# Kernel tuning notes

Measured on AMD Instinct MI355X. Metric: run time of the kernel, lower is better.

## Reference

```python
import jax, jax.numpy as jnp
import numpy as np


def _gaussian_orthogonal_random_matrix(nb_rows, nb_cols, seed=0):
    rng = np.random.default_rng(seed)
    blocks = []
    n_full = nb_rows // nb_cols
    for _ in range(n_full):
        q, _ = np.linalg.qr(rng.standard_normal((nb_cols, nb_cols)).astype(np.float64))
        blocks.append(q.T)
    rem = nb_rows - n_full * nb_cols
    if rem > 0:
        q, _ = np.linalg.qr(rng.standard_normal((nb_cols, nb_cols)).astype(np.float64))
        blocks.append(q.T[:rem])
    final = np.concatenate(blocks, axis=0)
    # scaling == 0: row multipliers are norms of gaussian rows
    multiplier = np.linalg.norm(rng.standard_normal((nb_rows, nb_cols)), axis=1)
    return (multiplier[:, None] * final).astype(np.float32)


def setup_inputs() -> dict:
    key = jax.random.key(0)
    kq, kk, kv = jax.random.split(key, 3)
    B, H, N, D = 4, 16, 4096, 64
    M = 256  # nb_features
    return {
        "q": jax.random.normal(kq, (B, H, N, D), dtype=jnp.float32),
        "k": jax.random.normal(kk, (B, H, N, D), dtype=jnp.float32),
        "v": jax.random.normal(kv, (B, H, N, D), dtype=jnp.float32),
        "projection_matrix": jnp.asarray(_gaussian_orthogonal_random_matrix(M, D)),
    }


def _softmax_kernel(data, proj, is_query, eps=1e-4):
    # data: [b,h,n,d], proj: [m,d]
    d = data.shape[-1]
    m = proj.shape[0]
    data_normalizer = d ** -0.25
    ratio = m ** -0.5
    data_dash = jnp.einsum('bhnd,md->bhnm', data_normalizer * data, proj)
    diag_data = jnp.sum(data * data, axis=-1, keepdims=True) * 0.5 * (data_normalizer ** 2)
    if is_query:
        mx = jnp.max(data_dash, axis=-1, keepdims=True)
    else:
        mx = jnp.max(data_dash, axis=(-2, -1), keepdims=True)
    mx = jax.lax.stop_gradient(mx)
    return ratio * (jnp.exp(data_dash - diag_data - mx) + eps)


def _linear_attention(q, k, v):
    # q,k: [b,h,n,m]; v: [b,h,n,e]
    k_cumsum = k.sum(axis=-2)                              # [b,h,m]
    d_inv = 1.0 / jnp.einsum('bhnm,bhm->bhn', q, k_cumsum)  # [b,h,n]
    context = jnp.einsum('bhnm,bhne->bhme', k, v)          # [b,h,m,e]
    return jnp.einsum('bhme,bhnm,bhn->bhne', context, q, d_inv)


def reference(q, k, v, projection_matrix):
    qp = _softmax_kernel(q, projection_matrix, is_query=True)
    kp = _softmax_kernel(k, projection_matrix, is_query=False)
    return _linear_attention(qp, kp, v)
```

## Files before the change

### kernel.cpp

```cpp
#include <hip/hip_runtime.h>
#include <math.h>

#define NSEQ  4096
#define DDIM  64
#define GH    64
#define NORMC 0.35355339059327373f
#define EPSC  1e-4f

typedef __bf16 bf16x8 __attribute__((ext_vector_type(8)));
typedef unsigned short u16x8 __attribute__((ext_vector_type(8)));
typedef float f32x4 __attribute__((ext_vector_type(4)));

__device__ __forceinline__ unsigned enc_f(float f) {
    unsigned b = __float_as_uint(f);
    return (b & 0x80000000u) ? ~b : (b | 0x80000000u);
}
__device__ __forceinline__ float dec_f(unsigned u) {
    return (u & 0x80000000u) ? __uint_as_float(u & 0x7FFFFFFFu) : __uint_as_float(~u);
}
__device__ __forceinline__ void split_hl(float f, unsigned short& h, unsigned short& l) {
    unsigned u = __float_as_uint(f);
    unsigned hb = u & 0xffff0000u;
    h = (unsigned short)(hb >> 16);
    l = (unsigned short)(__float_as_uint(f - __uint_as_float(hb)) >> 16);
}
__device__ __forceinline__ unsigned packsplit(float f) {
    unsigned short h, l;
    split_hl(f, h, l);
    return (unsigned)h | ((unsigned)l << 16);
}
__device__ __forceinline__ void unpack8(const unsigned* p, bf16x8& h, bf16x8& l) {
    u16x8 hh, ll;
#pragma unroll
    for (int j = 0; j < 8; j++) {
        hh[j] = (unsigned short)(p[j] & 0xffffu);
        ll[j] = (unsigned short)(p[j] >> 16);
    }
    h = __builtin_bit_cast(bf16x8, hh);
    l = __builtin_bit_cast(bf16x8, ll);
}
__device__ __forceinline__ bf16x8 ldfrag(const unsigned short* p) {
    return __builtin_bit_cast(bf16x8, *(const u16x8*)p);
}
__device__ __forceinline__ f32x4 zero4() { f32x4 z = {0.f, 0.f, 0.f, 0.f}; return z; }
__device__ __forceinline__ f32x4 mfma3(bf16x8 ah, bf16x8 al, bf16x8 bh, bf16x8 bl, f32x4 c) {
    c = __builtin_amdgcn_mfma_f32_16x16x32_bf16(ah, bh, c, 0, 0, 0);
    c = __builtin_amdgcn_mfma_f32_16x16x32_bf16(ah, bl, c, 0, 0, 0);
    c = __builtin_amdgcn_mfma_f32_16x16x32_bf16(al, bh, c, 0, 0, 0);
    return c;
}

template<int NSLICE>
__global__ __launch_bounds__(256, 2)
void kernA(const float* __restrict__ kk, const float* __restrict__ vv,
           const float* __restrict__ proj, float* __restrict__ Apart,
           float* __restrict__ Aspart, float* __restrict__ Svpart,
           unsigned* __restrict__ mxk)
{
    const int slices = (NSLICE == 1) ? 8 : NSLICE;
    const int slice = blockIdx.x;
    const int g     = blockIdx.y;
    const int t     = threadIdx.x;
    const int lane  = t & 63;
    const int wq    = t >> 6;
    const int li    = lane & 15;
    const int lg    = lane >> 4;

    __shared__ __align__(16) unsigned short Khi[2048];
    __shared__ __align__(16) unsigned short Klo[2048];
    __shared__ unsigned Vl[32 * 66];
    __shared__ unsigned Wl[4][32 * 66];
    __shared__ float diag[32];
    __shared__ float svred[4][64];
    __shared__ float mxred[4];

    bf16x8 pfh[4][2], pfl[4][2];
#pragma unroll
    for (int u = 0; u < 4; u++)
#pragma unroll
    for (int s = 0; s < 2; s++) {
        const float* pr = proj + (size_t)(wq * 64 + u * 16 + li) * DDIM + s * 32 + lg * 8;
        u16x8 hh, ll;
#pragma unroll
        for (int j = 0; j < 8; j++) {
            unsigned short h, l;
            split_hl(NORMC * pr[j], h, l);
            hh[j] = h; ll[j] = l;
        }
        pfh[u][s] = __builtin_bit_cast(bf16x8, hh);
        pfl[u][s] = __builtin_bit_cast(bf16x8, ll);
    }

    f32x4 cacc[4][4];
#pragma unroll
    for (int u = 0; u < 4; u++)
#pragma unroll
    for (int e = 0; e < 4; e++) cacc[u][e] = zero4();
    float as_loc[4] = {0.f, 0.f, 0.f, 0.f};
    float sv8[8] = {0.f,0.f,0.f,0.f,0.f,0.f,0.f,0.f};
    float mloc = -1e30f;

    const int stg_n = t >> 3;
    const int stg_c = t & 7;
    const int rows_per = NSEQ / slices;
    const int r_begin = slice * rows_per;

    for (int r0 = r_begin; r0 < r_begin + rows_per; r0 += 32) {
        {
            const float4* kb = (const float4*)(kk + ((size_t)g * NSEQ + r0 + stg_n) * DDIM + stg_c * 8);
            float4 a0 = kb[0], a1 = kb[1];
            float sq = a0.x*a0.x + a0.y*a0.y + a0.z*a0.z + a0.w*a0.w
                     + a1.x*a1.x + a1.y*a1.y + a1.z*a1.z + a1.w*a1.w;
            sq += __shfl_xor(sq, 1); sq += __shfl_xor(sq, 2); sq += __shfl_xor(sq, 4);
            if (stg_c == 0) diag[stg_n] = 0.0625f * sq;
            u16x8 h8, l8;
            {
                unsigned short h, l;
                split_hl(a0.x,h,l); h8[0]=h; l8[0]=l;
                split_hl(a0.y,h,l); h8[1]=h; l8[1]=l;
                split_hl(a0.z,h,l); h8[2]=h; l8[2]=l;
                split_hl(a0.w,h,l); h8[3]=h; l8[3]=l;
                split_hl(a1.x,h,l); h8[4]=h; l8[4]=l;
                split_hl(a1.y,h,l); h8[5]=h; l8[5]=l;
                split_hl(a1.z,h,l); h8[6]=h; l8[6]=l;
                split_hl(a1.w,h,l); h8[7]=h; l8[7]=l;
            }
            int idx = stg_n * 64 + (stg_c ^ (stg_n & 7)) * 8;
            *(u16x8*)&Khi[idx] = h8;
            *(u16x8*)&Klo[idx] = l8;
            const float4* vb = (const float4*)(vv + ((size_t)g * NSEQ + r0 + stg_n) * DDIM + stg_c * 8);
            float4 b0 = vb[0], b1 = vb[1];
            sv8[0]+=b0.x; sv8[1]+=b0.y; sv8[2]+=b0.z; sv8[3]+=b0.w;
            sv8[4]+=b1.x; sv8[5]+=b1.y; sv8[6]+=b1.z; sv8[7]+=b1.w;
            unsigned* vd = &Vl[stg_n * 66 + stg_c * 8];
            vd[0]=packsplit(b0.x); vd[1]=packsplit(b0.y); vd[2]=packsplit(b0.z); vd[3]=packsplit(b0.w);
            vd[4]=packsplit(b1.x); vd[5]=packsplit(b1.y); vd[6]=packsplit(b1.z); vd[7]=packsplit(b1.w);
        }
        __syncthreads();
        f32x4 dacc[2][4];
#pragma unroll
        for (int tt = 0; tt < 2; tt++)
#pragma unroll
        for (int u = 0; u < 4; u++) dacc[tt][u] = zero4();
#pragma unroll
        for (int tt = 0; tt < 2; tt++)
#pragma unroll
        for (int s = 0; s < 2; s++) {
            int idx = (tt * 16 + li) * 64 + ((s * 4 + lg) ^ (li & 7)) * 8;
            bf16x8 ah = ldfrag(&Khi[idx]);
            bf16x8 al = ldfrag(&Klo[idx]);
#pragma unroll
            for (int u = 0; u < 4; u++) dacc[tt][u] = mfma3(ah, al, pfh[u][s], pfl[u][s], dacc[tt][u]);
        }
#pragma unroll
        for (int tt = 0; tt < 2; tt++)
#pragma unroll
        for (int u = 0; u < 4; u++)
#pragma unroll
        for (int r = 0; r < 4; r++) {
            float dash = dacc[tt][u][r];
            mloc = fmaxf(mloc, dash);
            float w = __expf(dash - diag[tt * 16 + lg * 4 + r]);
            as_loc[u] += w;
            Wl[wq][(tt * 16 + lg * 4 + r) * 66 + u * 16 + li] = packsplit(w);
        }
        bf16x8 vh[4], vl2[4];
#pragma unroll
        for (int u2 = 0; u2 < 4; u2++) {
            unsigned vx[8];
            const unsigned* vr = &Vl[(lg * 8) * 66 + u2 * 16 + li];
#pragma unroll
            for (int j = 0; j < 8; j++) vx[j] = vr[j * 66];
            unpack8(vx, vh[u2], vl2[u2]);
        }
#pragma unroll
        for (int u = 0; u < 4; u++) {
            unsigned aw[8];
            const unsigned* wr = &Wl[wq][(lg * 8) * 66 + u * 16 + li];
#pragma unroll
            for (int j = 0; j < 8; j++) aw[j] = wr[j * 66];
            bf16x8 wh, wl_;
            unpack8(aw, wh, wl_);
#pragma unroll
            for (int u2 = 0; u2 < 4; u2++) cacc[u][u2] = mfma3(wh, wl_, vh[u2], vl2[u2], cacc[u][u2]);
        }
        __syncthreads();
    }

#pragma unroll
    for (int j = 0; j < 8; j++) {
        float s = sv8[j];
        s += __shfl_xor(s, 8); s += __shfl_xor(s, 16); s += __shfl_xor(s, 32);
        sv8[j] = s;
    }
    if (lane < 8) {
#pragma unroll
        for (int j = 0; j < 8; j++) svred[wq][lane * 8 + j] = sv8[j];
    }
    float mm = mloc;
#pragma unroll
    for (int off = 32; off >= 1; off >>= 1) mm = fmaxf(mm, __shfl_xor(mm, off));
    if (lane == 0) mxred[wq] = mm;
#pragma unroll
    for (int u = 0; u < 4; u++) {
        float a = as_loc[u];
        a += __shfl_xor(a, 16); a += __shfl_xor(a, 32);
        as_loc[u] = a;
    }
    __syncthreads();
    if (t == 0) {
        float m4 = fmaxf(fmaxf(mxred[0], mxred[1]), fmaxf(mxred[2], mxred[3]));
        atomicMax(mxk + g, enc_f(m4));
    }
    if (t < 64) {
        float s = svred[0][t] + svred[1][t] + svred[2][t] + svred[3][t];
        if (NSLICE == 1) atomicAdd(&Svpart[(size_t)g * 64 + t], s);
        else             Svpart[((size_t)g * NSLICE + slice) * 64 + t] = s;
    }
    if (lane < 16) {
#pragma unroll
        for (int u = 0; u < 4; u++) {
            int m = wq * 64 + u * 16 + lane;
            if (NSLICE == 1) atomicAdd(&Aspart[(size_t)g * 256 + m], as_loc[u]);
            else             Aspart[((size_t)g * NSLICE + slice) * 256 + m] = as_loc[u];
        }
    }
    if (NSLICE == 1) {
        float* Ad = Apart + (size_t)g * (256 * 64);
#pragma unroll
        for (int u = 0; u < 4; u++)
#pragma unroll
        for (int u2 = 0; u2 < 4; u2++)
#pragma unroll
        for (int r = 0; r < 4; r++)
            atomicAdd(&Ad[(wq * 64 + u * 16 + lg * 4 + r) * 64 + u2 * 16 + li], cacc[u][u2][r]);
    } else {
        float* Ad = Apart + ((size_t)g * NSLICE + slice) * (256 * 64);
#pragma unroll
        for (int u = 0; u < 4; u++)
#pragma unroll
        for (int u2 = 0; u2 < 4; u2++)
#pragma unroll
        for (int r = 0; r < 4; r++)
            Ad[(wq * 64 + u * 16 + lg * 4 + r) * 64 + u2 * 16 + li] = cacc[u][u2][r];
    }
}

__global__ __launch_bounds__(256)
void kernB(const float* __restrict__ Apart, const float* __restrict__ Aspart,
           const float* __restrict__ Svpart, const unsigned* __restrict__ mxk,
           float* __restrict__ ctx, float* __restrict__ ksum, int nslice)
{
    const int b = blockIdx.x;
    const int g = blockIdx.y;
    const int t = threadIdx.x;
    __shared__ float svh[64];
    float emx = __expf(-dec_f(mxk[g]));
    if (t < 64) {
        float s = 0.f;
        for (int sb = 0; sb < nslice; sb++) s += Svpart[((size_t)g * nslice + sb) * 64 + t];
        svh[t] = s;
    }
    if (b == 0) {
        float as_s = 0.f;
        for (int sb = 0; sb < nslice; sb++) as_s += Aspart[((size_t)g * nslice + sb) * 256 + t];
        ksum[(size_t)g * 256 + t] = emx * as_s + EPSC * (float)NSEQ;
    }
    __syncthreads();
    int idx4 = b * 256 + t;
    const f32x4* Ap = (const f32x4*)Apart;
    f32x4 s = zero4();
    for (int sb = 0; sb < nslice; sb++) s += Ap[((size_t)g * nslice + sb) * 4096 + idx4];
    int e0 = (idx4 * 4) & 63;
    f32x4 o;
    o[0] = emx * s[0] + EPSC * svh[e0];
    o[1] = emx * s[1] + EPSC * svh[e0 + 1];
    o[2] = emx * s[2] + EPSC * svh[e0 + 2];
    o[3] = emx * s[3] + EPSC * svh[e0 + 3];
    ((f32x4*)ctx)[(size_t)g * 4096 + idx4] = o;
}

__global__ __launch_bounds__(256, 2)
void kernC(const float* __restrict__ qq, const float* __restrict__ proj,
           const float* __restrict__ ctx, const float* __restrict__ ksum,
           float* __restrict__ outp)
{
    const int slice = blockIdx.x;
    const int g     = blockIdx.y;
    const int t     = threadIdx.x;
    const int lane  = t & 63;
    const int wq    = t >> 6;
    const int li    = lane & 15;
    const int lg    = lane >> 4;

    __shared__ __align__(16) unsigned short Qhi[2048];
    __shared__ __align__(16) unsigned short Qlo[2048];
    __shared__ uint4 wbuf[4][544];
    __shared__ float diag[32];
    __shared__ float rmax4[4][32];
    __shared__ float comb[32];
    __shared__ float denp[4][32];
    __shared__ float denc[32];

    bf16x8 pfh[4][2], pfl[4][2];
#pragma unroll
    for (int u = 0; u < 4; u++)
#pragma unroll
    for (int s = 0; s < 2; s++) {
        const float* pr = proj + (size_t)(wq * 64 + u * 16 + li) * DDIM + s * 32 + lg * 8;
        u16x8 hh, ll;
#pragma unroll
        for (int j = 0; j < 8; j++) {
            unsigned short h, l;
            split_hl(NORMC * pr[j], h, l);
            hh[j] = h; ll[j] = l;
        }
        pfh[u][s] = __builtin_bit_cast(bf16x8, hh);
        pfl[u][s] = __builtin_bit_cast(bf16x8, ll);
    }
    bf16x8 cfh[4][2], cfl[4][2];
#pragma unroll
    for (int u2 = 0; u2 < 4; u2++)
#pragma unroll
    for (int s = 0; s < 2; s++) {
        u16x8 hh, ll;
#pragma unroll
        for (int j = 0; j < 8; j++) {
            unsigned short h, l;
            split_hl(ctx[((size_t)g * 256 + wq * 64 + s * 32 + lg * 8 + j) * 64 + u2 * 16 + li], h, l);
            hh[j] = h; ll[j] = l;
        }
        cfh[u2][s] = __builtin_bit_cast(bf16x8, hh);
        cfl[u2][s] = __builtin_bit_cast(bf16x8, ll);
    }
    float ksm[4];
#pragma unroll
    for (int u = 0; u < 4; u++) ksm[u] = ksum[(size_t)g * 256 + wq * 64 + u * 16 + li];

    unsigned short* qh = (unsigned short*)&wbuf[wq][0];
    unsigned short* ql = qh + 2048;
    float* ob = (float*)&wbuf[wq][0];

    const int stg_n = t >> 3;
    const int stg_c = t & 7;
    const int r_begin = slice * (NSEQ / 16);

    for (int r0 = r_begin; r0 < r_begin + NSEQ / 16; r0 += 32) {
        {
            const float4* qb = (const float4*)(qq + ((size_t)g * NSEQ + r0 + stg_n) * DDIM + stg_c * 8);
            float4 a0 = qb[0], a1 = qb[1];
            float sq = a0.x*a0.x + a0.y*a0.y + a0.z*a0.z + a0.w*a0.w
                     + a1.x*a1.x + a1.y*a1.y + a1.z*a1.z + a1.w*a1.w;
            sq += __shfl_xor(sq, 1); sq += __shfl_xor(sq, 2); sq += __shfl_xor(sq, 4);
            if (stg_c == 0) diag[stg_n] = 0.0625f * sq;
            u16x8 h8, l8;
            {
                unsigned short h, l;
                split_hl(a0.x,h,l); h8[0]=h; l8[0]=l;
                split_hl(a0.y,h,l); h8[1]=h; l8[1]=l;
                split_hl(a0.z,h,l); h8[2]=h; l8[2]=l;
                split_hl(a0.w,h,l); h8[3]=h; l8[3]=l;
                split_hl(a1.x,h,l); h8[4]=h; l8[4]=l;
                split_hl(a1.y,h,l); h8[5]=h; l8[5]=l;
                split_hl(a1.z,h,l); h8[6]=h; l8[6]=l;
                split_hl(a1.w,h,l); h8[7]=h; l8[7]=l;
            }
            int idx = stg_n * 64 + (stg_c ^ (stg_n & 7)) * 8;
            *(u16x8*)&Qhi[idx] = h8;
            *(u16x8*)&Qlo[idx] = l8;
        }
        __syncthreads();
        f32x4 dacc[2][4];
#pragma unroll
        for (int tt = 0; tt < 2; tt++)
#pragma unroll
        for (int u = 0; u < 4; u++) dacc[tt][u] = zero4();
#pragma unroll
        for (int tt = 0; tt < 2; tt++)
#pragma unroll
        for (int s = 0; s < 2; s++) {
            int idx = (tt * 16 + li) * 64 + ((s * 4 + lg) ^ (li & 7)) * 8;
            bf16x8 ah = ldfrag(&Qhi[idx]);
            bf16x8 al = ldfrag(&Qlo[idx]);
#pragma unroll
            for (int u = 0; u < 4; u++) dacc[tt][u] = mfma3(ah, al, pfh[u][s], pfl[u][s], dacc[tt][u]);
        }
#pragma unroll
        for (int tt = 0; tt < 2; tt++)
#pragma unroll
        for (int r = 0; r < 4; r++) {
            float v = fmaxf(fmaxf(dacc[tt][0][r], dacc[tt][1][r]),
                            fmaxf(dacc[tt][2][r], dacc[tt][3][r]));
            v = fmaxf(v, __shfl_xor(v, 1));
            v = fmaxf(v, __shfl_xor(v, 2));
            v = fmaxf(v, __shfl_xor(v, 4));
            v = fmaxf(v, __shfl_xor(v, 8));
            if (li == 0) rmax4[wq][tt * 16 + lg * 4 + r] = v;
        }
        __syncthreads();
        if (t < 32) comb[t] = diag[t] + fmaxf(fmaxf(rmax4[0][t], rmax4[1][t]),
                                              fmaxf(rmax4[2][t], rmax4[3][t]));
        __syncthreads();
        float dl[2][4] = {{0.f,0.f,0.f,0.f},{0.f,0.f,0.f,0.f}};
#pragma unroll
        for (int tt = 0; tt < 2; tt++) {
            float cb[4];
#pragma unroll
            for (int r = 0; r < 4; r++) cb[r] = comb[tt * 16 + lg * 4 + r];
#pragma unroll
            for (int u = 0; u < 4; u++)
#pragma unroll
            for (int r = 0; r < 4; r++) {
                float qp = __expf(dacc[tt][u][r] - cb[r]) + EPSC;
                dl[tt][r] += qp * ksm[u];
                int n = tt * 16 + lg * 4 + r;
                int m = u * 16 + li;
                int idx = n * 64 + (((m >> 3) ^ (n & 7)) << 3) + (m & 7);
                unsigned short h, l;
                split_hl(qp, h, l);
                qh[idx] = h;
                ql[idx] = l;
            }
        }
#pragma unroll
        for (int tt = 0; tt < 2; tt++)
#pragma unroll
        for (int r = 0; r < 4; r++) {
            float v = dl[tt][r];
            v += __shfl_xor(v, 1); v += __shfl_xor(v, 2);
            v += __shfl_xor(v, 4); v += __shfl_xor(v, 8);
            if (li == 0) denp[wq][tt * 16 + lg * 4 + r] = v;
        }
        __syncthreads();
        if (t < 32) denc[t] = denp[0][t] + denp[1][t] + denp[2][t] + denp[3][t];
        f32x4 oacc[2][4];
#pragma unroll
        for (int tt = 0; tt < 2; tt++)
#pragma unroll
        for (int u2 = 0; u2 < 4; u2++) oacc[tt][u2] = zero4();
#pragma unroll
        for (int s = 0; s < 2; s++)
#pragma unroll
        for (int tt = 0; tt < 2; tt++) {
            int n = tt * 16 + li;
            int idx = n * 64 + ((s * 4 + lg) ^ (n & 7)) * 8;
            bf16x8 ah = ldfrag(&qh[idx]);
            bf16x8 al = ldfrag(&ql[idx]);
#pragma unroll
            for (int u2 = 0; u2 < 4; u2++)
                oacc[tt][u2] = mfma3(ah, al, cfh[u2][s], cfl[u2][s], oacc[tt][u2]);
        }
#pragma unroll
        for (int tt = 0; tt < 2; tt++)
#pragma unroll
        for (int u2 = 0; u2 < 4; u2++)
#pragma unroll
        for (int r = 0; r < 4; r++)
            ob[(tt * 16 + lg * 4 + r) * 68 + u2 * 16 + li] = oacc[tt][u2][r];
        __syncthreads();
        {
            float dinv = 1.0f / denc[stg_n];
            float o[8];
#pragma unroll
            for (int j = 0; j < 8; j++) {
                float s = 0.f;
#pragma unroll
                for (int w4 = 0; w4 < 4; w4++)
                    s += ((const float*)&wbuf[w4][0])[stg_n * 68 + stg_c * 8 + j];
                o[j] = s * dinv;
            }
            float4 o0 = {o[0], o[1], o[2], o[3]};
            float4 o1 = {o[4], o[5], o[6], o[7]};
            float* op = outp + ((size_t)g * NSEQ + r0 + stg_n) * DDIM + stg_c * 8;
            ((float4*)op)[0] = o0;
            ((float4*)op)[1] = o1;
        }
        __syncthreads();
    }
}

extern "C" void kernel_launch(void* const* d_in, const int* in_sizes, int n_in,
                              void* d_out, int out_size, void* d_ws, size_t ws_size,
                              hipStream_t stream)
{
    const float* q    = (const float*)d_in[0];
    const float* k    = (const float*)d_in[1];
    const float* v    = (const float*)d_in[2];
    const float* proj = (const float*)d_in[3];
    float* outp = (float*)d_out;

    size_t per_ns = (size_t)GH * 16384 + (size_t)GH * 256 + (size_t)GH * 64;
    size_t fixed  = (size_t)GH * 16384 + (size_t)GH * 256;
    size_t need16 = 256 + 4 * (16 * per_ns + fixed);
    size_t need8  = 256 + 4 * (8 * per_ns + fixed);
    int ns = (ws_size >= need16) ? 16 : ((ws_size >= need8) ? 8 : 1);

    unsigned* mxk = (unsigned*)d_ws;
    float* Apart  = (float*)((char*)d_ws + 256);
    float* Aspart = Apart  + (size_t)GH * ns * 16384;
    float* Svpart = Aspart + (size_t)GH * ns * 256;
    float* ctx    = Svpart + (size_t)GH * ns * 64;
    float* ksum   = ctx    + (size_t)GH * 16384;

    if (ns == 16) {
        hipMemsetAsync(d_ws, 0, 256, stream);
        kernA<16><<<dim3(16, GH), 256, 0, stream>>>(k, v, proj, Apart, Aspart, Svpart, mxk);
    } else if (ns == 8) {
        hipMemsetAsync(d_ws, 0, 256, stream);
        kernA<8><<<dim3(8, GH), 256, 0, stream>>>(k, v, proj, Apart, Aspart, Svpart, mxk);
    } else {
        hipMemsetAsync(d_ws, 0, 256 + 4 * per_ns, stream);
        kernA<1><<<dim3(8, GH), 256, 0, stream>>>(k, v, proj, Apart, Aspart, Svpart, mxk);
    }
    kernB<<<dim3(16, GH), 256, 0, stream>>>(Apart, Aspart, Svpart, mxk, ctx, ksum, ns);
    kernC<<<dim3(16, GH), 256, 0, stream>>>(q, proj, ctx, ksum, outp);
}
```

Measured before the change: 222.7 us.

## Transpose V staging, keep W in registers, shrink LDS and merge kernC syncs

In kernA, V is stored in LDS transposed as separate hi/lo bf16 planes so MFMA fragments can be loaded with vector reads. The exp weights stay in registers as the B operand instead of passing through a per-wave LDS buffer. The context output is staged through LDS so global stores and atomics are coalesced float4s. In kernC, Q staging aliases the per-wave buffer, which reduces LDS and allows launch_bounds 4. Two barriers are removed by computing the row max and denominators inline, and the output padding changes from 68 to 65. The fallback path now uses 16 slices.

```diff
diff --git a/kernel.cpp b/kernel.cpp
--- a/kernel.cpp
+++ b/kernel.cpp
@@ -23,21 +23,6 @@
     unsigned hb = u & 0xffff0000u;
     h = (unsigned short)(hb >> 16);
     l = (unsigned short)(__float_as_uint(f - __uint_as_float(hb)) >> 16);
-}
-__device__ __forceinline__ unsigned packsplit(float f) {
-    unsigned short h, l;
-    split_hl(f, h, l);
-    return (unsigned)h | ((unsigned)l << 16);
-}
-__device__ __forceinline__ void unpack8(const unsigned* p, bf16x8& h, bf16x8& l) {
-    u16x8 hh, ll;
-#pragma unroll
-    for (int j = 0; j < 8; j++) {
-        hh[j] = (unsigned short)(p[j] & 0xffffu);
-        ll[j] = (unsigned short)(p[j] >> 16);
-    }
-    h = __builtin_bit_cast(bf16x8, hh);
-    l = __builtin_bit_cast(bf16x8, ll);
 }
 __device__ __forceinline__ bf16x8 ldfrag(const unsigned short* p) {
     return __builtin_bit_cast(bf16x8, *(const u16x8*)p);
@@ -57,7 +42,7 @@
            float* __restrict__ Aspart, float* __restrict__ Svpart,
            unsigned* __restrict__ mxk)
 {
-    const int slices = (NSLICE == 1) ? 8 : NSLICE;
+    const int slices = (NSLICE == 1) ? 16 : NSLICE;
     const int slice = blockIdx.x;
     const int g     = blockIdx.y;
     const int t     = threadIdx.x;
@@ -66,13 +51,14 @@
     const int li    = lane & 15;
     const int lg    = lane >> 4;
 
-    __shared__ __align__(16) unsigned short Khi[2048];
-    __shared__ __align__(16) unsigned short Klo[2048];
-    __shared__ unsigned Vl[32 * 66];
-    __shared__ unsigned Wl[4][32 * 66];
+    __shared__ __align__(16) unsigned short KV[8192];
     __shared__ float diag[32];
     __shared__ float svred[4][64];
     __shared__ float mxred[4];
+    unsigned short* Khi  = KV;
+    unsigned short* Klo  = KV + 2048;
+    unsigned short* Vthi = KV + 4096;
+    unsigned short* Vtlo = KV + 6144;
 
     bf16x8 pfh[4][2], pfl[4][2];
 #pragma unroll
@@ -93,9 +79,9 @@
 
     f32x4 cacc[4][4];
 #pragma unroll
-    for (int u = 0; u < 4; u++)
-#pragma unroll
-    for (int e = 0; e < 4; e++) cacc[u][e] = zero4();
+    for (int a = 0; a < 4; a++)
+#pragma unroll
+    for (int b = 0; b < 4; b++) cacc[a][b] = zero4();
     float as_loc[4] = {0.f, 0.f, 0.f, 0.f};
     float sv8[8] = {0.f,0.f,0.f,0.f,0.f,0.f,0.f,0.f};
     float mloc = -1e30f;
@@ -104,6 +90,7 @@
     const int stg_c = t & 7;
     const int rows_per = NSEQ / slices;
     const int r_begin = slice * rows_per;
+    const int vks = ((stg_n >> 2) & 3) * 8 + (stg_n >> 4) * 4 + (stg_n & 3);
 
     for (int r0 = r_begin; r0 < r_begin + rows_per; r0 += 32) {
         {
@@ -130,11 +117,16 @@
             *(u16x8*)&Klo[idx] = l8;
             const float4* vb = (const float4*)(vv + ((size_t)g * NSEQ + r0 + stg_n) * DDIM + stg_c * 8);
             float4 b0 = vb[0], b1 = vb[1];
-            sv8[0]+=b0.x; sv8[1]+=b0.y; sv8[2]+=b0.z; sv8[3]+=b0.w;
-            sv8[4]+=b1.x; sv8[5]+=b1.y; sv8[6]+=b1.z; sv8[7]+=b1.w;
-            unsigned* vd = &Vl[stg_n * 66 + stg_c * 8];
-            vd[0]=packsplit(b0.x); vd[1]=packsplit(b0.y); vd[2]=packsplit(b0.z); vd[3]=packsplit(b0.w);
-            vd[4]=packsplit(b1.x); vd[5]=packsplit(b1.y); vd[6]=packsplit(b1.z); vd[7]=packsplit(b1.w);
+            float ve[8] = {b0.x,b0.y,b0.z,b0.w,b1.x,b1.y,b1.z,b1.w};
+#pragma unroll
+            for (int j = 0; j < 8; j++) {
+                sv8[j] += ve[j];
+                unsigned short h, l;
+                split_hl(ve[j], h, l);
+                int e = stg_c * 8 + j;
+                Vthi[e * 32 + vks] = h;
+                Vtlo[e * 32 + vks] = l;
+            }
         }
         __syncthreads();
         f32x4 dacc[2][4];
@@ -162,27 +154,30 @@
             mloc = fmaxf(mloc, dash);
             float w = __expf(dash - diag[tt * 16 + lg * 4 + r]);
             as_loc[u] += w;
-            Wl[wq][(tt * 16 + lg * 4 + r) * 66 + u * 16 + li] = packsplit(w);
-        }
-        bf16x8 vh[4], vl2[4];
+            dacc[tt][u][r] = w;
+        }
+        u16x8 whh[4], wll[4];
+#pragma unroll
+        for (int u = 0; u < 4; u++)
+#pragma unroll
+        for (int jj = 0; jj < 8; jj++) {
+            unsigned short h, l;
+            split_hl(dacc[jj >> 2][u][jj & 3], h, l);
+            whh[u][jj] = h; wll[u][jj] = l;
+        }
+        bf16x8 avh[4], avl[4];
 #pragma unroll
         for (int u2 = 0; u2 < 4; u2++) {
-            unsigned vx[8];
-            const unsigned* vr = &Vl[(lg * 8) * 66 + u2 * 16 + li];
-#pragma unroll
-            for (int j = 0; j < 8; j++) vx[j] = vr[j * 66];
-            unpack8(vx, vh[u2], vl2[u2]);
+            avh[u2] = ldfrag(&Vthi[(u2 * 16 + li) * 32 + lg * 8]);
+            avl[u2] = ldfrag(&Vtlo[(u2 * 16 + li) * 32 + lg * 8]);
         }
 #pragma unroll
         for (int u = 0; u < 4; u++) {
-            unsigned aw[8];
-            const unsigned* wr = &Wl[wq][(lg * 8) * 66 + u * 16 + li];
-#pragma unroll
-            for (int j = 0; j < 8; j++) aw[j] = wr[j * 66];
-            bf16x8 wh, wl_;
-            unpack8(aw, wh, wl_);
-#pragma unroll
-            for (int u2 = 0; u2 < 4; u2++) cacc[u][u2] = mfma3(wh, wl_, vh[u2], vl2[u2], cacc[u][u2]);
+            bf16x8 bh = __builtin_bit_cast(bf16x8, whh[u]);
+            bf16x8 bl = __builtin_bit_cast(bf16x8, wll[u]);
+#pragma unroll
+            for (int u2 = 0; u2 < 4; u2++)
+                cacc[u2][u] = mfma3(avh[u2], avl[u2], bh, bl, cacc[u2][u]);
         }
         __syncthreads();
     }
@@ -225,24 +220,28 @@
             else             Aspart[((size_t)g * NSLICE + slice) * 256 + m] = as_loc[u];
         }
     }
-    if (NSLICE == 1) {
-        float* Ad = Apart + (size_t)g * (256 * 64);
-#pragma unroll
-        for (int u = 0; u < 4; u++)
+    float* tb = (float*)KV + wq * 1024;
+    float* Ad = (NSLICE == 1) ? (Apart + (size_t)g * 16384)
+                              : (Apart + ((size_t)g * NSLICE + slice) * 16384);
+    for (int u = 0; u < 4; u++) {
 #pragma unroll
         for (int u2 = 0; u2 < 4; u2++)
 #pragma unroll
         for (int r = 0; r < 4; r++)
-            atomicAdd(&Ad[(wq * 64 + u * 16 + lg * 4 + r) * 64 + u2 * 16 + li], cacc[u][u2][r]);
-    } else {
-        float* Ad = Apart + ((size_t)g * NSLICE + slice) * (256 * 64);
-#pragma unroll
-        for (int u = 0; u < 4; u++)
-#pragma unroll
-        for (int u2 = 0; u2 < 4; u2++)
-#pragma unroll
-        for (int r = 0; r < 4; r++)
-            Ad[(wq * 64 + u * 16 + lg * 4 + r) * 64 + u2 * 16 + li] = cacc[u][u2][r];
+            tb[li * 64 + ((((u2 << 2) | lg) ^ (li & 7)) << 2) + r] = cacc[u2][u][r];
+#pragma unroll
+        for (int j = 0; j < 4; j++) {
+            int row16 = j * 4 + lg;
+            int swz = li ^ (row16 & 7);
+            f32x4 val = *(const f32x4*)&tb[row16 * 64 + swz * 4];
+            float* dst = Ad + (wq * 64 + u * 16) * 64 + j * 256 + lane * 4;
+            if (NSLICE == 1) {
+                atomicAdd(dst + 0, val[0]); atomicAdd(dst + 1, val[1]);
+                atomicAdd(dst + 2, val[2]); atomicAdd(dst + 3, val[3]);
+            } else {
+                *(f32x4*)dst = val;
+            }
+        }
     }
 }
 
@@ -280,7 +279,7 @@
     ((f32x4*)ctx)[(size_t)g * 4096 + idx4] = o;
 }
 
-__global__ __launch_bounds__(256, 2)
+__global__ __launch_bounds__(256, 4)
 void kernC(const float* __restrict__ qq, const float* __restrict__ proj,
            const float* __restrict__ ctx, const float* __restrict__ ksum,
            float* __restrict__ outp)
@@ -293,14 +292,16 @@
     const int li    = lane & 15;
     const int lg    = lane >> 4;
 
-    __shared__ __align__(16) unsigned short Qhi[2048];
-    __shared__ __align__(16) unsigned short Qlo[2048];
-    __shared__ uint4 wbuf[4][544];
+    __shared__ __align__(16) unsigned wbuf[4][2176];
     __shared__ float diag[32];
     __shared__ float rmax4[4][32];
-    __shared__ float comb[32];
     __shared__ float denp[4][32];
-    __shared__ float denc[32];
+
+    unsigned short* Qhi = (unsigned short*)&wbuf[0][0];
+    unsigned short* Qlo = Qhi + 2048;
+    unsigned short* qh  = (unsigned short*)&wbuf[wq][0];
+    unsigned short* ql  = qh + 2048;
+    float* ob = (float*)&wbuf[wq][0];
 
     bf16x8 pfh[4][2], pfl[4][2];
 #pragma unroll
@@ -336,10 +337,6 @@
     float ksm[4];
 #pragma unroll
     for (int u = 0; u < 4; u++) ksm[u] = ksum[(size_t)g * 256 + wq * 64 + u * 16 + li];
-
-    unsigned short* qh = (unsigned short*)&wbuf[wq][0];
-    unsigned short* ql = qh + 2048;
-    float* ob = (float*)&wbuf[wq][0];
 
     const int stg_n = t >> 3;
     const int stg_c = t & 7;
@@ -398,15 +395,16 @@
             if (li == 0) rmax4[wq][tt * 16 + lg * 4 + r] = v;
         }
         __syncthreads();
-        if (t < 32) comb[t] = diag[t] + fmaxf(fmaxf(rmax4[0][t], rmax4[1][t]),
-                                              fmaxf(rmax4[2][t], rmax4[3][t]));
-        __syncthreads();
         float dl[2][4] = {{0.f,0.f,0.f,0.f},{0.f,0.f,0.f,0.f}};
 #pragma unroll
         for (int tt = 0; tt < 2; tt++) {
             float cb[4];
 #pragma unroll
-            for (int r = 0; r < 4; r++) cb[r] = comb[tt * 16 + lg * 4 + r];
+            for (int r = 0; r < 4; r++) {
+                int n = tt * 16 + lg * 4 + r;
+                cb[r] = diag[n] + fmaxf(fmaxf(rmax4[0][n], rmax4[1][n]),
+                                        fmaxf(rmax4[2][n], rmax4[3][n]));
+            }
 #pragma unroll
             for (int u = 0; u < 4; u++)
 #pragma unroll
@@ -431,8 +429,6 @@
             v += __shfl_xor(v, 4); v += __shfl_xor(v, 8);
             if (li == 0) denp[wq][tt * 16 + lg * 4 + r] = v;
         }
-        __syncthreads();
-        if (t < 32) denc[t] = denp[0][t] + denp[1][t] + denp[2][t] + denp[3][t];
         f32x4 oacc[2][4];
 #pragma unroll
         for (int tt = 0; tt < 2; tt++)
@@ -456,17 +452,18 @@
         for (int u2 = 0; u2 < 4; u2++)
 #pragma unroll
         for (int r = 0; r < 4; r++)
-            ob[(tt * 16 + lg * 4 + r) * 68 + u2 * 16 + li] = oacc[tt][u2][r];
+            ob[(tt * 16 + lg * 4 + r) * 65 + u2 * 16 + li] = oacc[tt][u2][r];
         __syncthreads();
         {
-            float dinv = 1.0f / denc[stg_n];
+            float den = denp[0][stg_n] + denp[1][stg_n] + denp[2][stg_n] + denp[3][stg_n];
+            float dinv = 1.0f / den;
             float o[8];
 #pragma unroll
             for (int j = 0; j < 8; j++) {
                 float s = 0.f;
 #pragma unroll
                 for (int w4 = 0; w4 < 4; w4++)
-                    s += ((const float*)&wbuf[w4][0])[stg_n * 68 + stg_c * 8 + j];
+                    s += ((const float*)&wbuf[w4][0])[stg_n * 65 + stg_c * 8 + j];
                 o[j] = s * dinv;
             }
             float4 o0 = {o[0], o[1], o[2], o[3]};
@@ -510,7 +507,7 @@
         kernA<8><<<dim3(8, GH), 256, 0, stream>>>(k, v, proj, Apart, Aspart, Svpart, mxk);
     } else {
         hipMemsetAsync(d_ws, 0, 256 + 4 * per_ns, stream);
-        kernA<1><<<dim3(8, GH), 256, 0, stream>>>(k, v, proj, Apart, Aspart, Svpart, mxk);
+        kernA<1><<<dim3(16, GH), 256, 0, stream>>>(k, v, proj, Apart, Aspart, Svpart, mxk);
     }
     kernB<<<dim3(16, GH), 256, 0, stream>>>(Apart, Aspart, Svpart, mxk, ctx, ksum, ns);
     kernC<<<dim3(16, GH), 256, 0, stream>>>(q, proj, ctx, ksum, outp);
```

Result: slower. 405.0 us (+81.8%).
